# Kernel optimization log

Measured on AMD Instinct MI355X. Metric: run time of the kernel, lower is better.

The kernel has to match this reference:

```python
import jax, jax.numpy as jnp
import numpy as np

DIM = 512      # conv channels == B axis of token tensor
DEPTH = 16     # C axis of token tensor, used as conv depth D
HW = 64        # H = W


def _dwconv3d(inp, w, b, pad):
    # inp: (1, DIM, D, H, W); w: (DIM, 1, k, k, k); depthwise via feature_group_count
    out = jax.lax.conv_general_dilated(
        inp, w,
        window_strides=(1, 1, 1),
        padding=[(pad, pad)] * 3,
        dimension_numbers=("NCDHW", "OIDHW", "NCDHW"),
        feature_group_count=inp.shape[1],
    )
    return out + b[None, :, None, None, None]


def setup_inputs() -> dict:
    key = jax.random.key(0)
    ks = jax.random.split(key, 7)
    x = jax.random.normal(ks[0], (1, DIM, HW * HW, DEPTH), dtype=jnp.float32)
    # depthwise Conv3d weights: (out_ch=DIM, in_ch/groups=1, k, k, k)
    def wscale(k):
        return 1.0 / np.sqrt(k ** 3)  # kaiming-uniform-ish fan_in scale
    w7 = jax.random.normal(ks[1], (DIM, 1, 7, 7, 7), dtype=jnp.float32) * wscale(7)
    b7 = jax.random.normal(ks[2], (DIM,), dtype=jnp.float32) * 0.01
    w5 = jax.random.normal(ks[3], (DIM, 1, 5, 5, 5), dtype=jnp.float32) * wscale(5)
    b5 = jax.random.normal(ks[4], (DIM,), dtype=jnp.float32) * 0.01
    w3 = jax.random.normal(ks[5], (DIM, 1, 3, 3, 3), dtype=jnp.float32) * wscale(3)
    b3 = jax.random.normal(ks[6], (DIM,), dtype=jnp.float32) * 0.01
    return {"x": x, "w7": w7, "b7": b7, "w5": w5, "b5": b5,
            "w3": w3, "b3": b3, "H": HW, "W": HW}


def reference(x, w7, b7, w5, b5, w3, b3, H, W):
    # x: (1, B, N, C) with B==DIM, N==H*W
    _, B, N, C = x.shape
    # torch view(B, C, H, W).unsqueeze(0): pure row-major reinterpretation
    cnn_feat = x.reshape(1, B, C, H, W)  # (1, DIM, D, H, W)
    out = (
        _dwconv3d(cnn_feat, w7, b7, 3)
        + cnn_feat
        + _dwconv3d(cnn_feat, w5, b5, 2)
        + _dwconv3d(cnn_feat, w3, b3, 1)
    )
    # flatten(3).transpose(2, 3): (1, B, C, H*W) -> (1, B, H*W, C)
    out = out.reshape(1, B, C, H * W).transpose(0, 1, 3, 2)
    return out
```

## Files before the change

kernel.cpp:

```cpp
#include <hip/hip_runtime.h>

typedef _Float16 f16;
typedef _Float16 f16x8 __attribute__((ext_vector_type(8)));
typedef float    f32x4 __attribute__((ext_vector_type(4)));
typedef unsigned int   u32;
typedef unsigned short u16;

#define NCH   512
#define ND    16
#define NH    64
#define NW    64
#define HT    16
#define ROWS  22
#define RST   88
#define PLANE 4096
#define CHVOL 65536
#define NFRAG 49
#define FRAG_U4_PER_CH (NFRAG * 64)

__device__ __forceinline__ u16 f16bits(float v) {
    return __builtin_bit_cast(u16, (f16)v);
}

__global__ void build_weights(const float* __restrict__ w7,
                              const float* __restrict__ b7,
                              const float* __restrict__ w5,
                              const float* __restrict__ b5,
                              const float* __restrict__ w3,
                              const float* __restrict__ b3,
                              uint4* __restrict__ wfrag,
                              float* __restrict__ beff)
{
    __shared__ float weff[7][7][7];
    const int ch = blockIdx.x;
    const int t  = threadIdx.x;

    for (int i = t; i < 343; i += 64) {
        const int kd = i / 49;
        const int r  = i - kd * 49;
        const int kh = r / 7;
        const int kw = r - kh * 7;
        float v = w7[ch * 343 + i];
        if (kd >= 1 && kd <= 5 && kh >= 1 && kh <= 5 && kw >= 1 && kw <= 5)
            v += w5[ch * 125 + (kd - 1) * 25 + (kh - 1) * 5 + (kw - 1)];
        if (kd >= 2 && kd <= 4 && kh >= 2 && kh <= 4 && kw >= 2 && kw <= 4)
            v += w3[ch * 27 + (kd - 2) * 9 + (kh - 2) * 3 + (kw - 2)];
        if (kd == 3 && kh == 3 && kw == 3) v += 1.0f;
        weff[kh][kd][kw] = v;
    }
    __syncthreads();

    const int n    = t & 15;
    const int quad = t >> 4;
    uint4* wp = wfrag + ch * FRAG_U4_PER_CH + t;
    for (int kh = 0; kh < 7; ++kh) {
        for (int kd = 0; kd < 7; ++kd) {
            u32 pk[4];
            #pragma unroll
            for (int p = 0; p < 4; ++p) {
                const int t0 = quad * 8 + 2 * p - n - 5;
                const u32 lo = ((unsigned)t0       < 7u) ? (u32)f16bits(weff[kh][kd][t0])     : 0u;
                const u32 hi = ((unsigned)(t0 + 1) < 7u) ? (u32)f16bits(weff[kh][kd][t0 + 1]) : 0u;
                pk[p] = lo | (hi << 16);
            }
            wp[(kh * 7 + kd) * 64] = make_uint4(pk[0], pk[1], pk[2], pk[3]);
        }
    }
    if (t == 0) beff[ch] = b7[ch] + b5[ch] + b3[ch];
}

template<int DILO, int DIHI, int G8>
__device__ __forceinline__ void conv_group(const u16* slab,
                                           const uint4* __restrict__ wfc,
                                           const uint4* bw0,
                                           int n, int quad, int w0, float bv,
                                           float* __restrict__ ob, int h0)
{
    f32x4 acc[8];
    #pragma unroll
    for (int t = 0; t < 8; ++t) acc[t] = (f32x4){bv, bv, bv, bv};

    uint4 bw[7];
    #pragma unroll
    for (int kd = 0; kd < 7; ++kd) bw[kd] = bw0[kd];

    #pragma unroll 1
    for (int kh = 0; kh < 7; ++kh) {
        uint4 bwn[7];
        const int khn = (kh < 6) ? kh + 1 : 6;
        #pragma unroll
        for (int kd = 0; kd < 7; ++kd) bwn[kd] = wfc[(khn * 7 + kd) * 64];

        const u16* arow = slab + (n + kh) * RST + w0 + quad * 8;
        #pragma unroll
        for (int di = DILO; di <= DIHI; ++di) {
            const f16x8 Af = *(const f16x8*)(arow + di * (ROWS * RST));
            #pragma unroll
            for (int kd = 0; kd < 7; ++kd) {
                const int dout = di - kd + 3 - G8;
                if (dout < 0 || dout > 7) continue;
                acc[dout] = __builtin_amdgcn_mfma_f32_16x16x32_f16(
                                Af, __builtin_bit_cast(f16x8, bw[kd]), acc[dout], 0, 0, 0);
            }
        }
        #pragma unroll
        for (int kd = 0; kd < 7; ++kd) bw[kd] = bwn[kd];
    }

    #pragma unroll
    for (int r = 0; r < 4; ++r) {
        const int h = h0 + quad * 4 + r;
        float* p = ob + (h * NW + w0 + n) * ND + G8;
        #pragma unroll
        for (int tg = 0; tg < 2; ++tg) {
            const float4 v = make_float4(acc[4 * tg + 0][r], acc[4 * tg + 1][r],
                                         acc[4 * tg + 2][r], acc[4 * tg + 3][r]);
            *(float4*)(p + 4 * tg) = v;
        }
    }
}

__global__ __launch_bounds__(512, 4)
void dwconv_mfma(const float* __restrict__ in,
                 const uint4* __restrict__ wfrag,
                 const float* __restrict__ beff,
                 float* __restrict__ out)
{
    __shared__ u16 slab[ND * ROWS * RST];

    const int b     = blockIdx.x;
    const int xcd   = b & 7;
    const int local = b >> 3;
    const int ch    = xcd * 64 + (local >> 2);
    const int ht    = local & 3;
    const int h0    = ht * HT;
    const int tid   = threadIdx.x;
    const int lane  = tid & 63;

    const uint4* __restrict__ wfc = wfrag + ch * FRAG_U4_PER_CH + lane;
    uint4 bw0[7];
    #pragma unroll
    for (int kd = 0; kd < 7; ++kd) bw0[kd] = wfc[kd * 64];
    const float bv = beff[ch];

    const float* __restrict__ inb = in + ch * CHVOL;

    for (int idx = tid; idx < ND * ROWS * 20; idx += 512) {
        const int di = idx / (ROWS * 20);
        const int rm = idx - di * (ROWS * 20);
        const int r  = rm / 20;
        const int c  = rm - r * 20;
        const int ih = h0 - 3 + r;
        u32 p0 = 0u, p1 = 0u;
        if ((unsigned)ih < (unsigned)NH && c >= 2 && c <= 17) {
            const float4 v = *(const float4*)(inb + di * PLANE + ih * NW + (c * 4 - 8));
            p0 = (u32)f16bits(v.x) | ((u32)f16bits(v.y) << 16);
            p1 = (u32)f16bits(v.z) | ((u32)f16bits(v.w) << 16);
        }
        *(uint2*)(slab + (di * ROWS + r) * RST + c * 4) = make_uint2(p0, p1);
    }
    __syncthreads();

    const int wv    = tid >> 6;
    const int wtile = wv & 3;
    const int g     = wv >> 1 & 0;
    (void)g;
    const int grp   = wv >> 2;
    const int w0    = wtile * 16;
    const int n     = lane & 15;
    const int quad  = lane >> 4;

    float* __restrict__ ob = out + ch * CHVOL;

    if (grp == 0)
        conv_group<0, 10, 0>(slab, wfc, bw0, n, quad, w0, bv, ob, h0);
    else
        conv_group<5, 15, 8>(slab, wfc, bw0, n, quad, w0, bv, ob, h0);
}

extern "C" void kernel_launch(void* const* d_in, const int* in_sizes, int n_in,
                              void* d_out, int out_size, void* d_ws, size_t ws_size,
                              hipStream_t stream)
{
    const float* x  = (const float*)d_in[0];
    const float* w7 = (const float*)d_in[1];
    const float* b7 = (const float*)d_in[2];
    const float* w5 = (const float*)d_in[3];
    const float* b5 = (const float*)d_in[4];
    const float* w3 = (const float*)d_in[5];
    const float* b3 = (const float*)d_in[6];
    float* outp = (float*)d_out;

    uint4* wfrag = (uint4*)d_ws;
    float* beff  = (float*)((char*)d_ws
                            + (size_t)NCH * FRAG_U4_PER_CH * sizeof(uint4));

    build_weights<<<NCH, 64, 0, stream>>>(w7, b7, w5, b5, w3, b3, wfrag, beff);
    dwconv_mfma<<<NCH * 4, 512, 0, stream>>>(x, wfrag, beff, outp);
}
```

Before: 397.8 us.

## Merge depth-split wave groups so each wave computes all 16 depth outputs

Previously eight waves split the 16 output depths into two halves, and each half reread overlapping input depths and reloaded the same weights. Now four waves per block each hold 16 accumulators and cover every depth, which removes the duplicated LDS reads and weight fetches (7x16 MFMAs minus edges, instead of two 11-depth passes). The slab row stride shrinks from 88 to 72 and its right-side padding is dropped, with an 8-element zero tail added for overreads. The cost is higher register pressure, so launch bounds drop to 256 threads and 3 blocks, which may lower occupancy and latency hiding.

```diff
diff --git a/kernel.cpp b/kernel.cpp
--- a/kernel.cpp
+++ b/kernel.cpp
@@ -12,11 +12,12 @@
 #define NW    64
 #define HT    16
 #define ROWS  22
-#define RST   88
+#define RST   72
 #define PLANE 4096
 #define CHVOL 65536
 #define NFRAG 49
 #define FRAG_U4_PER_CH (NFRAG * 64)
+#define SLAB_U16 (ND * ROWS * RST)
 
 __device__ __forceinline__ u16 f16bits(float v) {
     return __builtin_bit_cast(u16, (f16)v);
@@ -69,64 +70,13 @@
     if (t == 0) beff[ch] = b7[ch] + b5[ch] + b3[ch];
 }
 
-template<int DILO, int DIHI, int G8>
-__device__ __forceinline__ void conv_group(const u16* slab,
-                                           const uint4* __restrict__ wfc,
-                                           const uint4* bw0,
-                                           int n, int quad, int w0, float bv,
-                                           float* __restrict__ ob, int h0)
-{
-    f32x4 acc[8];
-    #pragma unroll
-    for (int t = 0; t < 8; ++t) acc[t] = (f32x4){bv, bv, bv, bv};
-
-    uint4 bw[7];
-    #pragma unroll
-    for (int kd = 0; kd < 7; ++kd) bw[kd] = bw0[kd];
-
-    #pragma unroll 1
-    for (int kh = 0; kh < 7; ++kh) {
-        uint4 bwn[7];
-        const int khn = (kh < 6) ? kh + 1 : 6;
-        #pragma unroll
-        for (int kd = 0; kd < 7; ++kd) bwn[kd] = wfc[(khn * 7 + kd) * 64];
-
-        const u16* arow = slab + (n + kh) * RST + w0 + quad * 8;
-        #pragma unroll
-        for (int di = DILO; di <= DIHI; ++di) {
-            const f16x8 Af = *(const f16x8*)(arow + di * (ROWS * RST));
-            #pragma unroll
-            for (int kd = 0; kd < 7; ++kd) {
-                const int dout = di - kd + 3 - G8;
-                if (dout < 0 || dout > 7) continue;
-                acc[dout] = __builtin_amdgcn_mfma_f32_16x16x32_f16(
-                                Af, __builtin_bit_cast(f16x8, bw[kd]), acc[dout], 0, 0, 0);
-            }
-        }
-        #pragma unroll
-        for (int kd = 0; kd < 7; ++kd) bw[kd] = bwn[kd];
-    }
-
-    #pragma unroll
-    for (int r = 0; r < 4; ++r) {
-        const int h = h0 + quad * 4 + r;
-        float* p = ob + (h * NW + w0 + n) * ND + G8;
-        #pragma unroll
-        for (int tg = 0; tg < 2; ++tg) {
-            const float4 v = make_float4(acc[4 * tg + 0][r], acc[4 * tg + 1][r],
-                                         acc[4 * tg + 2][r], acc[4 * tg + 3][r]);
-            *(float4*)(p + 4 * tg) = v;
-        }
-    }
-}
-
-__global__ __launch_bounds__(512, 4)
+__global__ __launch_bounds__(256, 3)
 void dwconv_mfma(const float* __restrict__ in,
                  const uint4* __restrict__ wfrag,
                  const float* __restrict__ beff,
                  float* __restrict__ out)
 {
-    __shared__ u16 slab[ND * ROWS * RST];
+    __shared__ u16 slab[SLAB_U16 + 8];
 
     const int b     = blockIdx.x;
     const int xcd   = b & 7;
@@ -138,44 +88,74 @@
     const int lane  = tid & 63;
 
     const uint4* __restrict__ wfc = wfrag + ch * FRAG_U4_PER_CH + lane;
-    uint4 bw0[7];
+    uint4 bw[7];
     #pragma unroll
-    for (int kd = 0; kd < 7; ++kd) bw0[kd] = wfc[kd * 64];
+    for (int kd = 0; kd < 7; ++kd) bw[kd] = wfc[kd * 64];
     const float bv = beff[ch];
 
     const float* __restrict__ inb = in + ch * CHVOL;
 
-    for (int idx = tid; idx < ND * ROWS * 20; idx += 512) {
-        const int di = idx / (ROWS * 20);
-        const int rm = idx - di * (ROWS * 20);
-        const int r  = rm / 20;
-        const int c  = rm - r * 20;
+    for (int idx = tid; idx < ND * ROWS * 18; idx += 256) {
+        const int di = idx / (ROWS * 18);
+        const int rm = idx - di * (ROWS * 18);
+        const int r  = rm / 18;
+        const int c  = rm - r * 18;
         const int ih = h0 - 3 + r;
         u32 p0 = 0u, p1 = 0u;
-        if ((unsigned)ih < (unsigned)NH && c >= 2 && c <= 17) {
+        if ((unsigned)ih < (unsigned)NH && c >= 2) {
             const float4 v = *(const float4*)(inb + di * PLANE + ih * NW + (c * 4 - 8));
             p0 = (u32)f16bits(v.x) | ((u32)f16bits(v.y) << 16);
             p1 = (u32)f16bits(v.z) | ((u32)f16bits(v.w) << 16);
         }
         *(uint2*)(slab + (di * ROWS + r) * RST + c * 4) = make_uint2(p0, p1);
     }
+    if (tid < 8) slab[SLAB_U16 + tid] = (u16)0;
     __syncthreads();
 
     const int wv    = tid >> 6;
-    const int wtile = wv & 3;
-    const int g     = wv >> 1 & 0;
-    (void)g;
-    const int grp   = wv >> 2;
-    const int w0    = wtile * 16;
+    const int w0    = wv * 16;
     const int n     = lane & 15;
     const int quad  = lane >> 4;
 
+    f32x4 acc[16];
+    #pragma unroll
+    for (int t = 0; t < 16; ++t) acc[t] = (f32x4){bv, bv, bv, bv};
+
+    #pragma unroll 1
+    for (int kh = 0; kh < 7; ++kh) {
+        uint4 bwn[7];
+        const int khn = (kh < 6) ? kh + 1 : 6;
+        #pragma unroll
+        for (int kd = 0; kd < 7; ++kd) bwn[kd] = wfc[(khn * 7 + kd) * 64];
+
+        const u16* arow = slab + (n + kh) * RST + w0 + quad * 8;
+        #pragma unroll
+        for (int di = 0; di < ND; ++di) {
+            const f16x8 Af = *(const f16x8*)(arow + di * (ROWS * RST));
+            #pragma unroll
+            for (int kd = 0; kd < 7; ++kd) {
+                const int dout = di - kd + 3;
+                if (dout < 0 || dout > 15) continue;
+                acc[dout] = __builtin_amdgcn_mfma_f32_16x16x32_f16(
+                                Af, __builtin_bit_cast(f16x8, bw[kd]), acc[dout], 0, 0, 0);
+            }
+        }
+        #pragma unroll
+        for (int kd = 0; kd < 7; ++kd) bw[kd] = bwn[kd];
+    }
+
     float* __restrict__ ob = out + ch * CHVOL;
-
-    if (grp == 0)
-        conv_group<0, 10, 0>(slab, wfc, bw0, n, quad, w0, bv, ob, h0);
-    else
-        conv_group<5, 15, 8>(slab, wfc, bw0, n, quad, w0, bv, ob, h0);
+    #pragma unroll
+    for (int r = 0; r < 4; ++r) {
+        const int h = h0 + quad * 4 + r;
+        float* p = ob + (h * NW + w0 + n) * ND;
+        #pragma unroll
+        for (int tg = 0; tg < 4; ++tg) {
+            const float4 v = make_float4(acc[4 * tg + 0][r], acc[4 * tg + 1][r],
+                                         acc[4 * tg + 2][r], acc[4 * tg + 3][r]);
+            *(float4*)(p + 4 * tg) = v;
+        }
+    }
 }
 
 extern "C" void kernel_launch(void* const* d_in, const int* in_sizes, int n_in,
@@ -196,5 +176,5 @@
                             + (size_t)NCH * FRAG_U4_PER_CH * sizeof(uint4));
 
     build_weights<<<NCH, 64, 0, stream>>>(w7, b7, w5, b5, w3, b3, wfrag, beff);
-    dwconv_mfma<<<NCH * 4, 512, 0, stream>>>(x, wfrag, beff, outp);
+    dwconv_mfma<<<NCH * 4, 256, 0, stream>>>(x, wfrag, beff, outp);
 }
```

New measurement: 335.1 us. -15.8%, faster.
